# Kernel optimization log

Measured on AMD Instinct MI355X. Metric: run time of the kernel, lower is better.

The kernel has to match this reference:

```python
import jax, jax.numpy as jnp
import numpy as np

B, C, IMG = 64, 3, 256
NUM_CLASSES = 4
PATCH = 8
H = IMG // PATCH        # 32: unfold kernel == stride (non-overlapping blocks)
NH = IMG // H           # 8 blocks per side
P = NH * NH             # 64 patches per image
TOPK = 16
AGE = 1.0               # self.age at forward time (updated only after outputs computed)


def _to_patches(x):
    # x: [b, c, IMG, IMG] -> [b, c, H, H, P] matching torch Unfold(kernel=H, stride=H)
    b, c = x.shape[:2]
    return x.reshape(b, c, NH, H, NH, H).transpose(0, 1, 3, 5, 2, 4).reshape(b, c, H, H, P)


def _from_patches(p):
    # inverse of _to_patches (torch Fold)
    b, c = p.shape[:2]
    return p.reshape(b, c, H, H, NH, NH).transpose(0, 1, 4, 2, 5, 3).reshape(b, c, IMG, IMG)


def _dice_loss(pred, tgt):
    # per-sample dice loss, as in AdaMix.dice_loss
    t = jax.nn.one_hot(tgt, NUM_CLASSES, axis=1, dtype=pred.dtype)   # [B, nc, H, W]
    s = jax.nn.softmax(pred, axis=1)
    inter = jnp.sum(s * t, axis=(2, 3))
    union = jnp.sum(s + t, axis=(2, 3))
    return 1.0 - (2.0 * inter / (union + 1e-5)).mean(axis=1)


def _mix_one(o_p, a_p, o_idx, a_idx, k):
    # o_p, a_p: [Ct, H, H, P]; replace the first k sorted original patches
    # with the first k sorted augmented patches.
    sel = (jnp.arange(P) < k)[None, None, None, :]
    src = jnp.where(sel, a_p[..., a_idx], o_p[..., o_idx])
    return o_p.at[..., o_idx].set(src)


def reference(oimage, aimage, olabel, alabel, oconf, aconf, prediction, cur_step):
    # self-paced curriculum (self_paced=True branch); mixing branch taken deterministically
    loss = _dice_loss(prediction, olabel)                    # [B]
    sp_mask = loss < AGE                                     # bool [B]
    sp_w = 1.0 - loss / (AGE + 1e-5)                         # [B]
    k = jnp.minimum(TOPK, jnp.abs(jnp.trunc(TOPK * sp_w)).astype(jnp.int32))

    # pack image (C) + label (1, as float) + conf (1) so one gather/scatter mixes all
    o_all = jnp.concatenate([oimage, olabel[:, None].astype(oimage.dtype), oconf[:, None]], axis=1)
    a_all = jnp.concatenate([aimage, alabel[:, None].astype(aimage.dtype), aconf[:, None]], axis=1)
    o_p = _to_patches(o_all)                                 # [B, C+2, H, H, P]
    a_p = _to_patches(a_all)

    omean = o_p[:, C + 1].mean(axis=(1, 2))                  # [B, P] per-patch conf means
    amean = a_p[:, C + 1].mean(axis=(1, 2))
    # torch.sort(descending=sp_mask) for original, descending=not sp_mask for augmented
    sign = jnp.where(sp_mask, -1.0, 1.0)[:, None]
    o_idx = jnp.argsort(sign * omean, axis=1)
    a_idx = jnp.argsort(-sign * amean, axis=1)

    mixed = jax.vmap(_mix_one)(o_p, a_p, o_idx, a_idx, k)
    out = _from_patches(mixed)
    return out[:, :C], out[:, C].astype(jnp.int32), out[:, C + 1]


def setup_inputs() -> dict:
    key = jax.random.key(0)
    k1, k2, k3, k4, k5, k6, k7 = jax.random.split(key, 7)
    return {
        "oimage": jax.random.normal(k1, (B, C, IMG, IMG), dtype=jnp.float32),
        "aimage": jax.random.normal(k2, (B, C, IMG, IMG), dtype=jnp.float32),
        "olabel": jax.random.randint(k3, (B, IMG, IMG), 0, NUM_CLASSES, dtype=jnp.int32),
        "alabel": jax.random.randint(k4, (B, IMG, IMG), 0, NUM_CLASSES, dtype=jnp.int32),
        "oconf": jax.random.uniform(k5, (B, IMG, IMG), dtype=jnp.float32),
        "aconf": jax.random.uniform(k6, (B, IMG, IMG), dtype=jnp.float32),
        "prediction": jax.random.normal(k7, (B, NUM_CLASSES, IMG, IMG), dtype=jnp.float32),
        "cur_step": 100,
    }
```

## Files before the change

kernel.cpp:

```cpp
#include <hip/hip_runtime.h>
#include <hip/hip_bf16.h>

#define NB 64
#define NPIX 65536
#define NCLS 4
#define NPATCH 64
#define TOPK 16


__global__ void k_zero(float* __restrict__ acc) {
    int i = blockIdx.x * 256 + threadIdx.x;
    if (i < NB * 12) acc[i] = 0.f;
}

__device__ __forceinline__ void px_acc(float p0, float p1, float p2, float p3, int t,
                                       float& i0, float& i1, float& i2, float& i3,
                                       float& s0, float& s1, float& s2, float& s3,
                                       float& c0, float& c1, float& c2, float& c3) {
    float m  = fmaxf(fmaxf(p0, p1), fmaxf(p2, p3));
    float e0 = expf(p0 - m), e1 = expf(p1 - m), e2 = expf(p2 - m), e3 = expf(p3 - m);
    float inv = 1.f / (e0 + e1 + e2 + e3);
    float q0 = e0 * inv, q1 = e1 * inv, q2 = e2 * inv, q3 = e3 * inv;
    s0 += q0; s1 += q1; s2 += q2; s3 += q3;
    i0 += (t == 0) ? q0 : 0.f;
    i1 += (t == 1) ? q1 : 0.f;
    i2 += (t == 2) ? q2 : 0.f;
    i3 += (t == 3) ? q3 : 0.f;
    c0 += (float)(t == 0); c1 += (float)(t == 1);
    c2 += (float)(t == 2); c3 += (float)(t == 3);
}

__global__ void k_dice(const float* __restrict__ pred, const int* __restrict__ lab,
                       float* __restrict__ acc) {
    const int b     = blockIdx.x;
    const int chunk = blockIdx.y;
    const int tid   = threadIdx.x;
    const float* pb = pred + (size_t)b * NCLS * NPIX;
    const int*   lb = lab  + (size_t)b * NPIX;
    const float4* P0 = (const float4*)pb;
    const float4* P1 = (const float4*)(pb + NPIX);
    const float4* P2 = (const float4*)(pb + 2 * NPIX);
    const float4* P3 = (const float4*)(pb + 3 * NPIX);
    const int4*   L  = (const int4*)lb;

    float i0 = 0, i1 = 0, i2 = 0, i3 = 0;
    float s0 = 0, s1 = 0, s2 = 0, s3 = 0;
    float c0 = 0, c1 = 0, c2 = 0, c3 = 0;

    #pragma unroll
    for (int it = 0; it < 8; ++it) {
        int i4 = chunk * 2048 + it * 256 + tid;
        float4 a = P0[i4], b4 = P1[i4], c4 = P2[i4], d4 = P3[i4];
        int4 lv = L[i4];
        px_acc(a.x, b4.x, c4.x, d4.x, lv.x, i0, i1, i2, i3, s0, s1, s2, s3, c0, c1, c2, c3);
        px_acc(a.y, b4.y, c4.y, d4.y, lv.y, i0, i1, i2, i3, s0, s1, s2, s3, c0, c1, c2, c3);
        px_acc(a.z, b4.z, c4.z, d4.z, lv.z, i0, i1, i2, i3, s0, s1, s2, s3, c0, c1, c2, c3);
        px_acc(a.w, b4.w, c4.w, d4.w, lv.w, i0, i1, i2, i3, s0, s1, s2, s3, c0, c1, c2, c3);
    }

    float vals[12] = {i0, i1, i2, i3, s0, s1, s2, s3, c0, c1, c2, c3};
    #pragma unroll
    for (int j = 0; j < 12; ++j) {
        float v = vals[j];
        #pragma unroll
        for (int off = 32; off > 0; off >>= 1) v += __shfl_down(v, off, 64);
        if ((tid & 63) == 0) atomicAdd(&acc[b * 12 + j], v);
    }
}

__global__ void k_conf(const float* __restrict__ oconf, const float* __restrict__ aconf,
                       float* __restrict__ omean, float* __restrict__ amean) {
    const int br    = blockIdx.x;
    const int which = blockIdx.y;
    const int b     = blockIdx.z;
    const int tid   = threadIdx.x;
    const float* src = which ? aconf : oconf;
    const float4* s4 = (const float4*)(src + (size_t)b * NPIX + br * 32 * 256);
    const int f4c = tid & 63;
    const int r0  = tid >> 6;

    float s = 0.f;
    #pragma unroll
    for (int it = 0; it < 8; ++it) {
        float4 v = s4[(r0 + it * 4) * 64 + f4c];
        s += v.x + v.y + v.z + v.w;
    }
    __shared__ float psum[8];
    if (tid < 8) psum[tid] = 0.f;
    __syncthreads();
    atomicAdd(&psum[f4c >> 3], s);
    __syncthreads();
    if (tid < 8) {
        float* dst = which ? amean : omean;
        dst[b * 64 + br * 8 + tid] = psum[tid] * (1.0f / 1024.0f);
    }
}

__global__ void k_sortmap(const float* __restrict__ acc,
                          const float* __restrict__ omean, const float* __restrict__ amean,
                          int* __restrict__ srcmap) {
    const int b   = blockIdx.x;
    const int tid = threadIdx.x;
    const float* ac = acc + b * 12;

    float dice = 0.f;
    #pragma unroll
    for (int c = 0; c < 4; ++c) {
        float inter = ac[c], sumS = ac[4 + c], cnt = ac[8 + c];
        dice += 2.f * inter / (sumS + cnt + 1e-5f);
    }
    float loss = 1.f - dice * 0.25f;
    bool  sp   = loss < 1.0f;
    float sign = sp ? -1.f : 1.f;
    float spw  = 1.f - loss / (1.0f + 1e-5f);
    int   k    = min(TOPK, (int)fabsf(truncf((float)TOPK * spw)));

    __shared__ float keyo[64], keya[64];
    __shared__ int   oidx[64], aidx[64];
    float ko = sign  * omean[b * 64 + tid];
    float ka = -sign * amean[b * 64 + tid];
    keyo[tid] = ko; keya[tid] = ka;
    __syncthreads();

    int ro = 0, ra = 0;
    for (int j = 0; j < 64; ++j) {
        float kj = keyo[j];
        ro += (kj < ko || (kj == ko && j < tid)) ? 1 : 0;
        float k2 = keya[j];
        ra += (k2 < ka || (k2 == ka && j < tid)) ? 1 : 0;
    }
    oidx[ro] = tid;
    aidx[ra] = tid;
    __syncthreads();

    int pos = oidx[tid];
    srcmap[b * 64 + pos] = (tid < k) ? aidx[tid] : -1;
}

__global__ void k_assemble(const float* __restrict__ oimage, const float* __restrict__ aimage,
                           const int* __restrict__ olabel, const int* __restrict__ alabel,
                           const float* __restrict__ oconf, const float* __restrict__ aconf,
                           const int* __restrict__ srcmap, float* __restrict__ out) {
    const int b  = blockIdx.z;
    const int ch = blockIdx.y;
    const int f4 = blockIdx.x * 256 + threadIdx.x;
    const int pix = f4 << 2;
    const int y = pix >> 8, x = pix & 255;
    const int p = ((y >> 5) << 3) + (x >> 5);
    const int m = srcmap[(b << 6) + p];
    const bool aug = (m >= 0);
    int sy = y, sx = x;
    if (aug) { sy = ((m >> 3) << 5) + (y & 31); sx = ((m & 7) << 5) + (x & 31); }
    const int sidx4 = ((sy << 8) + sx) >> 2;
    const size_t bplane = (size_t)b << 16;

    if (ch < 3) {
        const size_t plane = (size_t)(b * 3 + ch) << 16;
        const float4* src = (const float4*)((aug ? aimage : oimage) + plane);
        ((float4*)(out + plane))[f4] = src[sidx4];
    } else if (ch == 3) {
        const int4* src = (const int4*)((aug ? alabel : olabel) + bplane);
        int4 v = src[sidx4];
        float4 w = make_float4((float)v.x, (float)v.y, (float)v.z, (float)v.w);
        ((float4*)(out + 12582912 + bplane))[f4] = w;
    } else {
        const float4* src = (const float4*)((aug ? aconf : oconf) + bplane);
        ((float4*)(out + 16777216 + bplane))[f4] = src[sidx4];
    }
}

extern "C" void kernel_launch(void* const* d_in, const int* in_sizes, int n_in,
                              void* d_out, int out_size, void* d_ws, size_t ws_size,
                              hipStream_t stream) {
    const float* oimage = (const float*)d_in[0];
    const float* aimage = (const float*)d_in[1];
    const int*   olabel = (const int*)d_in[2];
    const int*   alabel = (const int*)d_in[3];
    const float* oconf  = (const float*)d_in[4];
    const float* aconf  = (const float*)d_in[5];
    const float* pred   = (const float*)d_in[6];

    float* ws     = (float*)d_ws;
    float* acc    = ws;
    float* omean  = ws + 1024;
    float* amean  = ws + 5120;
    int*   srcmap = (int*)(ws + 9216);

    float* out = (float*)d_out;

    hipLaunchKernelGGL(k_zero,     dim3(3),           dim3(256), 0, stream, acc);
    hipLaunchKernelGGL(k_dice,     dim3(NB, 8),       dim3(256), 0, stream, pred, olabel, acc);
    hipLaunchKernelGGL(k_conf,     dim3(8, 2, NB),    dim3(256), 0, stream, oconf, aconf, omean, amean);
    hipLaunchKernelGGL(k_sortmap,  dim3(NB),          dim3(64),  0, stream, acc, omean, amean, srcmap);
    hipLaunchKernelGGL(k_assemble, dim3(64, 5, NB),   dim3(256), 0, stream,
                       oimage, aimage, olabel, alabel, oconf, aconf, srcmap, out);
}
```

Baseline: 301.2 us.

## Fuse dice and conf reductions into one launch, drop zeroing and global atomics

Merges the dice-loss reduction and the patch confidence-mean reduction into a single kernel that dispatches on block id, which removes the separate zeroing launch. Global atomics are replaced by per-block partial sums written to workspace and summed in the sort kernel. The dice work is split into 4x more blocks with fewer iterations each, and expf becomes __expf. The aim is to cut launch overhead and atomic contention and to raise parallelism, at the cost of slightly lower exp precision and a serial 32-element sum per batch in the sort kernel.

After: 255.1 us. 15.3% less time.

```diff
diff --git a/kernel.cpp b/kernel.cpp
--- a/kernel.cpp
+++ b/kernel.cpp
@@ -8,17 +8,12 @@
 #define TOPK 16
 
 
-__global__ void k_zero(float* __restrict__ acc) {
-    int i = blockIdx.x * 256 + threadIdx.x;
-    if (i < NB * 12) acc[i] = 0.f;
-}
-
 __device__ __forceinline__ void px_acc(float p0, float p1, float p2, float p3, int t,
                                        float& i0, float& i1, float& i2, float& i3,
                                        float& s0, float& s1, float& s2, float& s3,
                                        float& c0, float& c1, float& c2, float& c3) {
     float m  = fmaxf(fmaxf(p0, p1), fmaxf(p2, p3));
-    float e0 = expf(p0 - m), e1 = expf(p1 - m), e2 = expf(p2 - m), e3 = expf(p3 - m);
+    float e0 = __expf(p0 - m), e1 = __expf(p1 - m), e2 = __expf(p2 - m), e3 = __expf(p3 - m);
     float inv = 1.f / (e0 + e1 + e2 + e3);
     float q0 = e0 * inv, q1 = e1 * inv, q2 = e2 * inv, q3 = e3 * inv;
     s0 += q0; s1 += q1; s2 += q2; s3 += q3;
@@ -30,85 +25,98 @@
     c2 += (float)(t == 2); c3 += (float)(t == 3);
 }
 
-__global__ void k_dice(const float* __restrict__ pred, const int* __restrict__ lab,
-                       float* __restrict__ acc) {
-    const int b     = blockIdx.x;
-    const int chunk = blockIdx.y;
-    const int tid   = threadIdx.x;
-    const float* pb = pred + (size_t)b * NCLS * NPIX;
-    const int*   lb = lab  + (size_t)b * NPIX;
-    const float4* P0 = (const float4*)pb;
-    const float4* P1 = (const float4*)(pb + NPIX);
-    const float4* P2 = (const float4*)(pb + 2 * NPIX);
-    const float4* P3 = (const float4*)(pb + 3 * NPIX);
-    const int4*   L  = (const int4*)lb;
-
-    float i0 = 0, i1 = 0, i2 = 0, i3 = 0;
-    float s0 = 0, s1 = 0, s2 = 0, s3 = 0;
-    float c0 = 0, c1 = 0, c2 = 0, c3 = 0;
-
-    #pragma unroll
-    for (int it = 0; it < 8; ++it) {
-        int i4 = chunk * 2048 + it * 256 + tid;
-        float4 a = P0[i4], b4 = P1[i4], c4 = P2[i4], d4 = P3[i4];
-        int4 lv = L[i4];
-        px_acc(a.x, b4.x, c4.x, d4.x, lv.x, i0, i1, i2, i3, s0, s1, s2, s3, c0, c1, c2, c3);
-        px_acc(a.y, b4.y, c4.y, d4.y, lv.y, i0, i1, i2, i3, s0, s1, s2, s3, c0, c1, c2, c3);
-        px_acc(a.z, b4.z, c4.z, d4.z, lv.z, i0, i1, i2, i3, s0, s1, s2, s3, c0, c1, c2, c3);
-        px_acc(a.w, b4.w, c4.w, d4.w, lv.w, i0, i1, i2, i3, s0, s1, s2, s3, c0, c1, c2, c3);
-    }
-
-    float vals[12] = {i0, i1, i2, i3, s0, s1, s2, s3, c0, c1, c2, c3};
-    #pragma unroll
-    for (int j = 0; j < 12; ++j) {
-        float v = vals[j];
-        #pragma unroll
-        for (int off = 32; off > 0; off >>= 1) v += __shfl_down(v, off, 64);
-        if ((tid & 63) == 0) atomicAdd(&acc[b * 12 + j], v);
-    }
-}
-
-__global__ void k_conf(const float* __restrict__ oconf, const float* __restrict__ aconf,
-                       float* __restrict__ omean, float* __restrict__ amean) {
-    const int br    = blockIdx.x;
-    const int which = blockIdx.y;
-    const int b     = blockIdx.z;
-    const int tid   = threadIdx.x;
-    const float* src = which ? aconf : oconf;
-    const float4* s4 = (const float4*)(src + (size_t)b * NPIX + br * 32 * 256);
-    const int f4c = tid & 63;
-    const int r0  = tid >> 6;
-
-    float s = 0.f;
-    #pragma unroll
-    for (int it = 0; it < 8; ++it) {
-        float4 v = s4[(r0 + it * 4) * 64 + f4c];
-        s += v.x + v.y + v.z + v.w;
-    }
-    __shared__ float psum[8];
-    if (tid < 8) psum[tid] = 0.f;
-    __syncthreads();
-    atomicAdd(&psum[f4c >> 3], s);
-    __syncthreads();
-    if (tid < 8) {
-        float* dst = which ? amean : omean;
-        dst[b * 64 + br * 8 + tid] = psum[tid] * (1.0f / 1024.0f);
-    }
-}
-
-__global__ void k_sortmap(const float* __restrict__ acc,
+__global__ void k_stage1(const float* __restrict__ pred, const int* __restrict__ lab,
+                         const float* __restrict__ oconf, const float* __restrict__ aconf,
+                         float* __restrict__ part, float* __restrict__ omean,
+                         float* __restrict__ amean) {
+    __shared__ float smem[48];
+    const int bid = blockIdx.x;
+    const int tid = threadIdx.x;
+
+    if (bid < 2048) {
+        const int b     = bid >> 5;
+        const int chunk = bid & 31;
+        const float* pb = pred + (size_t)b * NCLS * NPIX;
+        const float4* P0 = (const float4*)pb;
+        const float4* P1 = (const float4*)(pb + NPIX);
+        const float4* P2 = (const float4*)(pb + 2 * NPIX);
+        const float4* P3 = (const float4*)(pb + 3 * NPIX);
+        const int4*   L  = (const int4*)(lab + (size_t)b * NPIX);
+
+        float i0 = 0, i1 = 0, i2 = 0, i3 = 0;
+        float s0 = 0, s1 = 0, s2 = 0, s3 = 0;
+        float c0 = 0, c1 = 0, c2 = 0, c3 = 0;
+
+        #pragma unroll
+        for (int it = 0; it < 2; ++it) {
+            int i4 = chunk * 512 + it * 256 + tid;
+            float4 a = P0[i4], b4 = P1[i4], c4 = P2[i4], d4 = P3[i4];
+            int4 lv = L[i4];
+            px_acc(a.x, b4.x, c4.x, d4.x, lv.x, i0, i1, i2, i3, s0, s1, s2, s3, c0, c1, c2, c3);
+            px_acc(a.y, b4.y, c4.y, d4.y, lv.y, i0, i1, i2, i3, s0, s1, s2, s3, c0, c1, c2, c3);
+            px_acc(a.z, b4.z, c4.z, d4.z, lv.z, i0, i1, i2, i3, s0, s1, s2, s3, c0, c1, c2, c3);
+            px_acc(a.w, b4.w, c4.w, d4.w, lv.w, i0, i1, i2, i3, s0, s1, s2, s3, c0, c1, c2, c3);
+        }
+
+        float vals[12] = {i0, i1, i2, i3, s0, s1, s2, s3, c0, c1, c2, c3};
+        const int wave = tid >> 6, lane = tid & 63;
+        #pragma unroll
+        for (int j = 0; j < 12; ++j) {
+            float v = vals[j];
+            #pragma unroll
+            for (int off = 32; off > 0; off >>= 1) v += __shfl_down(v, off, 64);
+            if (lane == 0) smem[wave * 12 + j] = v;
+        }
+        __syncthreads();
+        if (tid < 12)
+            part[(b * 32 + chunk) * 12 + tid] =
+                smem[tid] + smem[12 + tid] + smem[24 + tid] + smem[36 + tid];
+    } else {
+        const int cid   = bid - 2048;
+        const int br    = cid & 7;
+        const int which = (cid >> 3) & 1;
+        const int b     = cid >> 4;
+        const float* src = which ? aconf : oconf;
+        const float4* s4 = (const float4*)(src + (size_t)b * NPIX + br * 32 * 256);
+        const int f4c = tid & 63;
+        const int r0  = tid >> 6;
+
+        float s = 0.f;
+        #pragma unroll
+        for (int it = 0; it < 8; ++it) {
+            float4 v = s4[(r0 + it * 4) * 64 + f4c];
+            s += v.x + v.y + v.z + v.w;
+        }
+        if (tid < 8) smem[tid] = 0.f;
+        __syncthreads();
+        atomicAdd(&smem[f4c >> 3], s);
+        __syncthreads();
+        if (tid < 8) {
+            float* dst = which ? amean : omean;
+            dst[b * 64 + br * 8 + tid] = smem[tid] * (1.0f / 1024.0f);
+        }
+    }
+}
+
+__global__ void k_sortmap(const float* __restrict__ part,
                           const float* __restrict__ omean, const float* __restrict__ amean,
                           int* __restrict__ srcmap) {
     const int b   = blockIdx.x;
     const int tid = threadIdx.x;
-    const float* ac = acc + b * 12;
+
+    __shared__ float accs[12];
+    if (tid < 12) {
+        float s = 0.f;
+        #pragma unroll
+        for (int c = 0; c < 32; ++c) s += part[(b * 32 + c) * 12 + tid];
+        accs[tid] = s;
+    }
+    __syncthreads();
 
     float dice = 0.f;
     #pragma unroll
-    for (int c = 0; c < 4; ++c) {
-        float inter = ac[c], sumS = ac[4 + c], cnt = ac[8 + c];
-        dice += 2.f * inter / (sumS + cnt + 1e-5f);
-    }
+    for (int c = 0; c < 4; ++c)
+        dice += 2.f * accs[c] / (accs[4 + c] + accs[8 + c] + 1e-5f);
     float loss = 1.f - dice * 0.25f;
     bool  sp   = loss < 1.0f;
     float sign = sp ? -1.f : 1.f;
@@ -181,17 +189,16 @@
     const float* pred   = (const float*)d_in[6];
 
     float* ws     = (float*)d_ws;
-    float* acc    = ws;
-    float* omean  = ws + 1024;
-    float* amean  = ws + 5120;
-    int*   srcmap = (int*)(ws + 9216);
+    float* part   = ws;
+    float* omean  = ws + 24576;
+    float* amean  = ws + 28672;
+    int*   srcmap = (int*)(ws + 32768);
 
     float* out = (float*)d_out;
 
-    hipLaunchKernelGGL(k_zero,     dim3(3),           dim3(256), 0, stream, acc);
-    hipLaunchKernelGGL(k_dice,     dim3(NB, 8),       dim3(256), 0, stream, pred, olabel, acc);
-    hipLaunchKernelGGL(k_conf,     dim3(8, 2, NB),    dim3(256), 0, stream, oconf, aconf, omean, amean);
-    hipLaunchKernelGGL(k_sortmap,  dim3(NB),          dim3(64),  0, stream, acc, omean, amean, srcmap);
+    hipLaunchKernelGGL(k_stage1,   dim3(3072),        dim3(256), 0, stream,
+                       pred, olabel, oconf, aconf, part, omean, amean);
+    hipLaunchKernelGGL(k_sortmap,  dim3(NB),          dim3(64),  0, stream, part, omean, amean, srcmap);
     hipLaunchKernelGGL(k_assemble, dim3(64, 5, NB),   dim3(256), 0, stream,
                        oimage, aimage, olabel, alabel, oconf, aconf, srcmap, out);
 }
```
